# Performance work log

Measured on AMD Instinct MI355X. Metric: run time of the kernel, lower is better.

Reference implementation:

```python
import jax, jax.numpy as jnp
import numpy as np

B, S, D = 4, 2048, 768

def setup_inputs() -> dict:
    key = jax.random.key(0)
    ks = jax.random.split(key, 7)
    scale = 1.0 / np.sqrt(D)
    x = jax.random.normal(ks[0], (B, S, D), dtype=jnp.float32)
    Wq = jax.random.uniform(ks[1], (D, D), jnp.float32, -scale, scale)
    bq = jax.random.uniform(ks[2], (D,), jnp.float32, -scale, scale)
    Wk = jax.random.uniform(ks[3], (D, D), jnp.float32, -scale, scale)
    bk = jax.random.uniform(ks[4], (D,), jnp.float32, -scale, scale)
    Wv = jax.random.uniform(ks[5], (D, D), jnp.float32, -scale, scale)
    bv = jax.random.uniform(ks[6], (D,), jnp.float32, -scale, scale)
    return {"x": x, "Wq": Wq, "bq": bq, "Wk": Wk, "bk": bk, "Wv": Wv, "bv": bv}

def reference(x, Wq, bq, Wk, bk, Wv, bv):
    d = x.shape[-1]
    q = jnp.einsum('bsd,de->bse', x, Wq) + bq
    k = jnp.einsum('bsd,de->bse', x, Wk) + bk
    v = jnp.einsum('bsd,de->bse', x, Wv) + bv
    scores = jnp.einsum('bqd,bkd->bqk', q, k) / jnp.sqrt(jnp.asarray(d, x.dtype))
    attn = jax.nn.softmax(scores, axis=-1)  # [B,S,S]
    return jnp.einsum('bqk,bkd->bqd', attn, v)
```

## Files before the change

kernel.cpp:

```cpp
#include <hip/hip_runtime.h>
#include <hip/hip_bf16.h>


typedef __attribute__((ext_vector_type(8))) short short8;
typedef __attribute__((ext_vector_type(4))) short short4v;
typedef __attribute__((ext_vector_type(4))) float float4v;

static constexpr int B_ = 4, S_ = 2048, D_ = 768;
static constexpr int MS = B_ * S_;

__device__ inline short f2bf(float f) {
  __hip_bfloat16 h = __float2bfloat16(f);
  union { __hip_bfloat16 h; short s; } u; u.h = h; return u.s;
}

typedef const __attribute__((address_space(1))) unsigned int g_u32;
typedef __attribute__((address_space(3))) unsigned int l_u32;

__device__ __forceinline__ void glds16(const short* g, short* l) {
  __builtin_amdgcn_global_load_lds((g_u32*)g, (l_u32*)l, 16, 0, 0);
}

__global__ __launch_bounds__(256)
void cast_f32_bf16(const float* __restrict__ x, short* __restrict__ y, int n) {
  int i = (blockIdx.x * 256 + threadIdx.x) * 4;
  if (i + 3 < n) {
    float4v v = *(const float4v*)(x + i);
    short4v o;
    o.x = f2bf(v.x); o.y = f2bf(v.y); o.z = f2bf(v.z); o.w = f2bf(v.w);
    *(short4v*)(y + i) = o;
  }
}

__global__ void transpose_cast_w(const float* __restrict__ W0, const float* __restrict__ W1,
                                 const float* __restrict__ W2,
                                 short* __restrict__ T0, short* __restrict__ T1,
                                 short* __restrict__ T2) {
  const float* W = blockIdx.z == 0 ? W0 : (blockIdx.z == 1 ? W1 : W2);
  short* T = blockIdx.z == 0 ? T0 : (blockIdx.z == 1 ? T1 : T2);
  __shared__ float tile[32][33];
  int bx = blockIdx.x * 32, by = blockIdx.y * 32;
  int tx = threadIdx.x, ty = threadIdx.y;
  for (int r = ty; r < 32; r += 8)
    tile[r][tx] = W[(by + r) * D_ + bx + tx];
  __syncthreads();
  for (int r = ty; r < 32; r += 8)
    T[(bx + r) * D_ + by + tx] = f2bf(tile[tx][r]);
}

template<int EPI, int TM, int TN>
__global__ __launch_bounds__(256)
void gemm_bt(const short* __restrict__ A, const short* __restrict__ Bt,
             void* __restrict__ C0v, short* __restrict__ C1, short* __restrict__ C2,
             const float* __restrict__ bias0, const float* __restrict__ bias1,
             const float* __restrict__ bias2,
             int K, int lda, int ldb, int ldc,
             long sA, long sB, long sC, float scale) {
  constexpr int BMv = TM * 32, BNv = TN * 32;
  const int b = blockIdx.z;
  A += (long)b * sA;
  Bt += (long)b * sB;
  float* Cf = (float*)C0v + (long)b * sC;
  short* Cs = (short*)C0v + (long)b * sC;

  __shared__ short As[BMv * 64];
  __shared__ short Bs[BNv * 64];

  const int t = threadIdx.x;
  const int wave = t >> 6, lane = t & 63;
  const int lane16 = lane & 15, q = lane >> 4;
  const int m0 = blockIdx.y * BMv, n0 = blockIdx.x * BNv;
  const int wm = (wave >> 1) * (TM * 16), wn = (wave & 1) * (TN * 16);
  const int rsub = lane >> 3;
  const int g = (lane & 7) ^ rsub;

  auto stage = [&](int kk) {
#pragma unroll
    for (int i = wave; i < BMv / 8; i += 4)
      glds16(A + (long)(m0 + i * 8 + rsub) * lda + kk + g * 8, &As[i * 512]);
#pragma unroll
    for (int i = wave; i < BNv / 8; i += 4)
      glds16(Bt + (long)(n0 + i * 8 + rsub) * ldb + kk + g * 8, &Bs[i * 512]);
  };

  stage(0);

  float4v acc[TM][TN];
#pragma unroll
  for (int i = 0; i < TM; i++)
#pragma unroll
    for (int j = 0; j < TN; j++) acc[i][j] = {0.f, 0.f, 0.f, 0.f};

  constexpr int NRS = TM > TN ? TM : TN;
  float4v acc_rs[NRS];
#pragma unroll
  for (int i = 0; i < NRS; i++) acc_rs[i] = {0.f, 0.f, 0.f, 0.f};
  short8 ones;
#pragma unroll
  for (int e = 0; e < 8; e++) ones[e] = (short)0x3F80;

  for (int k0 = 0; k0 < K; k0 += 64) {
    __syncthreads();

    short8 af[2][TM], bfr[2][TN];
#pragma unroll
    for (int s = 0; s < 2; s++) {
#pragma unroll
      for (int i = 0; i < TM; i++) {
        int R = wm + i * 16 + lane16;
        af[s][i] = *(const short8*)&As[R * 64 + (((s * 4 + q) ^ (R & 7)) * 8)];
      }
#pragma unroll
      for (int j = 0; j < TN; j++) {
        int R = wn + j * 16 + lane16;
        bfr[s][j] = *(const short8*)&Bs[R * 64 + (((s * 4 + q) ^ (R & 7)) * 8)];
      }
    }
    __syncthreads();

    if (k0 + 64 < K) stage(k0 + 64);

#pragma unroll
    for (int s = 0; s < 2; s++) {
      if (EPI == 4) {
#pragma unroll
        for (int j = 0; j < TN; j++)
          acc_rs[j] = __builtin_amdgcn_mfma_f32_16x16x32_bf16(ones, bfr[s][j], acc_rs[j], 0, 0, 0);
      }
#pragma unroll
      for (int i = 0; i < TM; i++) {
#pragma unroll
        for (int j = 0; j < TN; j++)
          acc[i][j] = __builtin_amdgcn_mfma_f32_16x16x32_bf16(af[s][i], bfr[s][j], acc[i][j], 0, 0, 0);
      }
    }
  }

#pragma unroll
  for (int i = 0; i < TM; i++) {
    int mrow = m0 + wm + i * 16 + q * 4;
    if (EPI == 0) {
#pragma unroll
      for (int j = 0; j < TN; j++) {
        int ncol = n0 + wn + j * 16 + lane16;
        if (ncol < 1536) {
          short* dst = ncol < 768 ? Cs : C1;
          const float* bs = ncol < 768 ? bias0 : bias1;
          int c = ncol < 768 ? ncol : ncol - 768;
#pragma unroll
          for (int rr = 0; rr < 4; rr++)
            dst[(long)(mrow + rr) * 768 + c] = f2bf(acc[i][j][rr] + bs[c]);
        } else {
          int e = ncol - 1536;
          float bv = bias2[e];
          short4v o;
#pragma unroll
          for (int rr = 0; rr < 4; rr++) o[rr] = f2bf(acc[i][j][rr] + bv);
          *(short4v*)&C2[(long)e * MS + mrow] = o;
        }
      }
    } else {
#pragma unroll
      for (int j = 0; j < TN; j++) {
        int ncol = n0 + wn + j * 16 + lane16;
        float inv = 1.0f / acc_rs[j][0];
        float4v o;
#pragma unroll
        for (int rr = 0; rr < 4; rr++) o[rr] = acc[i][j][rr] * inv;
        *(float4v*)&Cf[(long)ncol * ldc + mrow] = o;
      }
    }
  }
}

template<int EPI>
__global__ __launch_bounds__(512, 2)
void gemm8p(const short* __restrict__ A, const short* __restrict__ Bt,
            void* __restrict__ C0v, short* __restrict__ C1, short* __restrict__ C2,
            const float* __restrict__ bias0, const float* __restrict__ bias1,
            const float* __restrict__ bias2,
            int K, int lda, int ldb, int ldc,
            long sA, long sB, long sC, float scale) {
  const int b = blockIdx.z;
  A += (long)b * sA;
  Bt += (long)b * sB;
  short* Cs = (short*)C0v + (long)b * sC;

  __shared__ short As[2][256 * 64];
  __shared__ short Bs[2][256 * 64];

  const int t = threadIdx.x;
  const int wave = t >> 6, lane = t & 63;
  const int lane16 = lane & 15, q = lane >> 4;
  const int xr = lane16 & 7;
  const int m0 = blockIdx.y * 256, n0 = blockIdx.x * 256;
  const int wm = (wave >> 2) * 128, wn = (wave & 3) * 64;
  const int rsub = lane >> 3;
  const int g = (lane & 7) ^ rsub;
  const int nt = K >> 6;

  auto stageA = [&](int u, int tt) {
    short* dst = &As[tt & 1][0];
    const short* src = A + tt * 64 + g * 8;
#pragma unroll
    for (int r = 0; r < 2; r++) {
      int row0 = u * 64 + r * 128 + wave * 8;
      glds16(src + (long)(m0 + row0 + rsub) * lda, dst + row0 * 64);
    }
  };
  auto stageB = [&](int u, int tt) {
    short* dst = &Bs[tt & 1][0];
    const short* src = Bt + tt * 64 + g * 8;
#pragma unroll
    for (int r = 0; r < 2; r++) {
      int idx = r * 8 + wave;
      int row0 = (idx >> 2) * 64 + u * 32 + (idx & 3) * 8;
      glds16(src + (long)(n0 + row0 + rsub) * ldb, dst + row0 * 64);
    }
  };

  float4v acc[8][4];
#pragma unroll
  for (int i = 0; i < 8; i++)
#pragma unroll
    for (int j = 0; j < 4; j++) acc[i][j] = {0.f, 0.f, 0.f, 0.f};

  stageA(0, 0); stageA(1, 0); stageB(0, 0); stageB(1, 0);
  if (nt > 1) { stageA(0, 1); stageB(0, 1); stageA(1, 1); }
  if (nt > 1) asm volatile("s_waitcnt vmcnt(6)" ::: "memory");
  else        asm volatile("s_waitcnt vmcnt(0)" ::: "memory");
  __builtin_amdgcn_s_barrier();

#pragma unroll 2
  for (int tt = 0; tt < nt; ++tt) {
    const short* Ab = &As[tt & 1][0];
    const short* Bb = &Bs[tt & 1][0];
    short8 a[4][2], b0[2][2], b1[2][2];

#pragma unroll
    for (int ii = 0; ii < 4; ii++) {
      int R = wm + ii * 16 + lane16;
#pragma unroll
      for (int s = 0; s < 2; s++)
        a[ii][s] = *(const short8*)&Ab[R * 64 + (((s * 4 + q) ^ xr) * 8)];
    }
#pragma unroll
    for (int jj = 0; jj < 2; jj++) {
      int R = wn + jj * 16 + lane16;
#pragma unroll
      for (int s = 0; s < 2; s++)
        b0[jj][s] = *(const short8*)&Bb[R * 64 + (((s * 4 + q) ^ xr) * 8)];
    }
    if (tt + 1 < nt) stageB(1, tt + 1);
    __builtin_amdgcn_s_barrier();
    asm volatile("s_waitcnt lgkmcnt(0)" ::: "memory");
    __builtin_amdgcn_sched_barrier(0);
    __builtin_amdgcn_s_setprio(1);
#pragma unroll
    for (int s = 0; s < 2; s++)
#pragma unroll
      for (int ii = 0; ii < 4; ii++)
#pragma unroll
        for (int jj = 0; jj < 2; jj++)
          acc[ii][jj] = __builtin_amdgcn_mfma_f32_16x16x32_bf16(a[ii][s], b0[jj][s], acc[ii][jj], 0, 0, 0);
    __builtin_amdgcn_s_setprio(0);
    __builtin_amdgcn_s_barrier();

#pragma unroll
    for (int jj = 0; jj < 2; jj++) {
      int R = wn + 32 + jj * 16 + lane16;
#pragma unroll
      for (int s = 0; s < 2; s++)
        b1[jj][s] = *(const short8*)&Bb[R * 64 + (((s * 4 + q) ^ xr) * 8)];
    }
    if (tt + 2 < nt) stageA(0, tt + 2);
    __builtin_amdgcn_s_barrier();
    asm volatile("s_waitcnt lgkmcnt(0)" ::: "memory");
    __builtin_amdgcn_sched_barrier(0);
    __builtin_amdgcn_s_setprio(1);
#pragma unroll
    for (int s = 0; s < 2; s++)
#pragma unroll
      for (int ii = 0; ii < 4; ii++)
#pragma unroll
        for (int jj = 0; jj < 2; jj++)
          acc[ii][2 + jj] = __builtin_amdgcn_mfma_f32_16x16x32_bf16(a[ii][s], b1[jj][s], acc[ii][2 + jj], 0, 0, 0);
    __builtin_amdgcn_s_setprio(0);
    __builtin_amdgcn_s_barrier();

#pragma unroll
    for (int ii = 0; ii < 4; ii++) {
      int R = wm + 64 + ii * 16 + lane16;
#pragma unroll
      for (int s = 0; s < 2; s++)
        a[ii][s] = *(const short8*)&Ab[R * 64 + (((s * 4 + q) ^ xr) * 8)];
    }
    if (tt + 2 < nt) stageB(0, tt + 2);
    __builtin_amdgcn_s_barrier();
    asm volatile("s_waitcnt lgkmcnt(0)" ::: "memory");
    __builtin_amdgcn_sched_barrier(0);
    __builtin_amdgcn_s_setprio(1);
#pragma unroll
    for (int s = 0; s < 2; s++)
#pragma unroll
      for (int ii = 0; ii < 4; ii++)
#pragma unroll
        for (int jj = 0; jj < 2; jj++)
          acc[4 + ii][2 + jj] = __builtin_amdgcn_mfma_f32_16x16x32_bf16(a[ii][s], b1[jj][s], acc[4 + ii][2 + jj], 0, 0, 0);
    __builtin_amdgcn_s_setprio(0);
    __builtin_amdgcn_s_barrier();

    if (tt + 2 < nt) stageA(1, tt + 2);
    __builtin_amdgcn_s_barrier();
    __builtin_amdgcn_s_setprio(1);
#pragma unroll
    for (int s = 0; s < 2; s++)
#pragma unroll
      for (int ii = 0; ii < 4; ii++)
#pragma unroll
        for (int jj = 0; jj < 2; jj++)
          acc[4 + ii][jj] = __builtin_amdgcn_mfma_f32_16x16x32_bf16(a[ii][s], b0[jj][s], acc[4 + ii][jj], 0, 0, 0);
    __builtin_amdgcn_s_setprio(0);
    if (tt + 2 < nt) asm volatile("s_waitcnt vmcnt(6)" ::: "memory");
    else             asm volatile("s_waitcnt vmcnt(0)" ::: "memory");
    __builtin_amdgcn_s_barrier();
  }

#pragma unroll
  for (int i = 0; i < 8; i++) {
    int mrow = m0 + wm + i * 16 + q * 4;
#pragma unroll
    for (int j = 0; j < 4; j++) {
      int ncol = n0 + wn + j * 16 + lane16;
#pragma unroll
      for (int rr = 0; rr < 4; rr++)
        Cs[(long)(mrow + rr) * ldc + ncol] = f2bf(__expf(acc[i][j][rr] * scale));
    }
  }
}

extern "C" void kernel_launch(void* const* d_in, const int* in_sizes, int n_in,
                              void* d_out, int out_size, void* d_ws, size_t ws_size,
                              hipStream_t stream) {
  const float* x  = (const float*)d_in[0];
  const float* Wq = (const float*)d_in[1];
  const float* bq = (const float*)d_in[2];
  const float* Wk = (const float*)d_in[3];
  const float* bk = (const float*)d_in[4];
  const float* Wv = (const float*)d_in[5];
  const float* bv = (const float*)d_in[6];
  float* out = (float*)d_out;

  short* Xb  = (short*)d_ws;
  short* WqT = Xb + (long)MS * D_;
  short* WkT = WqT + (long)D_ * D_;
  short* WvT = WkT + (long)D_ * D_;
  short* Qb  = WvT + (long)D_ * D_;
  short* Kb  = Qb + (long)MS * D_;
  short* Vt  = Kb + (long)MS * D_;
  short* Es  = Vt + (long)MS * D_;

  cast_f32_bf16<<<(MS * D_) / 1024, 256, 0, stream>>>(x, Xb, MS * D_);
  transpose_cast_w<<<dim3(24, 24, 3), dim3(32, 8), 0, stream>>>(Wq, Wk, Wv, WqT, WkT, WvT);

  gemm_bt<0, 4, 4><<<dim3(2304 / 128, MS / 128, 1), 256, 0, stream>>>(
      Xb, WqT, Qb, Kb, Vt, bq, bk, bv,
      D_, D_, D_, D_, 0, 0, 0, 1.0f);
  gemm8p<2><<<dim3(S_ / 256, S_ / 256, B_), 512, 0, stream>>>(
      Qb, Kb, Es, nullptr, nullptr, nullptr, nullptr, nullptr,
      D_, D_, D_, S_,
      (long)S_ * D_, (long)S_ * D_, (long)S_ * S_, 1.0f / sqrtf((float)D_));
  gemm_bt<4, 4, 4><<<dim3(S_ / 128, D_ / 128, B_), 256, 0, stream>>>(
      Vt, Es, out, nullptr, nullptr, nullptr, nullptr, nullptr,
      S_, MS, S_, D_,
      (long)S_, (long)S_ * S_, (long)S_ * D_, 1.0f);
}
```

Measured before the change: 196.5 us.

## Run PV GEMM on 256x256 pipelined kernel with split-K and combine pass

Replaces the 128x128 gemm_bt for the attention-times-V product with the 8-wave 256x256 pipelined gemm8p kernel. The key dimension is split in two halves across blockIdx.z to raise block count, and each half writes fp32 partials and row sums. A new pv_combine kernel adds the halves and normalizes by the summed row sums. This trades an extra fp32 partial buffer round-trip and an extra launch for higher MFMA efficiency in the big GEMM.

```diff
diff --git a/kernel.cpp b/kernel.cpp
--- a/kernel.cpp
+++ b/kernel.cpp
@@ -48,6 +48,20 @@
     T[(bx + r) * D_ + by + tx] = f2bf(tile[tx][r]);
 }
 
+__global__ __launch_bounds__(256)
+void pv_combine(const float* __restrict__ p1, const float* __restrict__ rs,
+                float* __restrict__ out) {
+  long i = ((long)blockIdx.x * 256 + threadIdx.x) * 4;
+  long qg = i / 768;
+  float inv = 1.0f / (rs[qg] + rs[8192 + qg]);
+  float4v a = *(const float4v*)(out + i);
+  float4v p = *(const float4v*)(p1 + i);
+  float4v o;
+#pragma unroll
+  for (int r = 0; r < 4; r++) o[r] = (a[r] + p[r]) * inv;
+  *(float4v*)(out + i) = o;
+}
+
 template<int EPI, int TM, int TN>
 __global__ __launch_bounds__(256)
 void gemm_bt(const short* __restrict__ A, const short* __restrict__ Bt,
@@ -60,7 +74,6 @@
   const int b = blockIdx.z;
   A += (long)b * sA;
   Bt += (long)b * sB;
-  float* Cf = (float*)C0v + (long)b * sC;
   short* Cs = (short*)C0v + (long)b * sC;
 
   __shared__ short As[BMv * 64];
@@ -91,14 +104,6 @@
 #pragma unroll
     for (int j = 0; j < TN; j++) acc[i][j] = {0.f, 0.f, 0.f, 0.f};
 
-  constexpr int NRS = TM > TN ? TM : TN;
-  float4v acc_rs[NRS];
-#pragma unroll
-  for (int i = 0; i < NRS; i++) acc_rs[i] = {0.f, 0.f, 0.f, 0.f};
-  short8 ones;
-#pragma unroll
-  for (int e = 0; e < 8; e++) ones[e] = (short)0x3F80;
-
   for (int k0 = 0; k0 < K; k0 += 64) {
     __syncthreads();
 
@@ -122,11 +127,6 @@
 
 #pragma unroll
     for (int s = 0; s < 2; s++) {
-      if (EPI == 4) {
-#pragma unroll
-        for (int j = 0; j < TN; j++)
-          acc_rs[j] = __builtin_amdgcn_mfma_f32_16x16x32_bf16(ones, bfr[s][j], acc_rs[j], 0, 0, 0);
-      }
 #pragma unroll
       for (int i = 0; i < TM; i++) {
 #pragma unroll
@@ -139,35 +139,23 @@
 #pragma unroll
   for (int i = 0; i < TM; i++) {
     int mrow = m0 + wm + i * 16 + q * 4;
-    if (EPI == 0) {
-#pragma unroll
-      for (int j = 0; j < TN; j++) {
-        int ncol = n0 + wn + j * 16 + lane16;
-        if (ncol < 1536) {
-          short* dst = ncol < 768 ? Cs : C1;
-          const float* bs = ncol < 768 ? bias0 : bias1;
-          int c = ncol < 768 ? ncol : ncol - 768;
-#pragma unroll
-          for (int rr = 0; rr < 4; rr++)
-            dst[(long)(mrow + rr) * 768 + c] = f2bf(acc[i][j][rr] + bs[c]);
-        } else {
-          int e = ncol - 1536;
-          float bv = bias2[e];
-          short4v o;
-#pragma unroll
-          for (int rr = 0; rr < 4; rr++) o[rr] = f2bf(acc[i][j][rr] + bv);
-          *(short4v*)&C2[(long)e * MS + mrow] = o;
-        }
-      }
-    } else {
-#pragma unroll
-      for (int j = 0; j < TN; j++) {
-        int ncol = n0 + wn + j * 16 + lane16;
-        float inv = 1.0f / acc_rs[j][0];
-        float4v o;
-#pragma unroll
-        for (int rr = 0; rr < 4; rr++) o[rr] = acc[i][j][rr] * inv;
-        *(float4v*)&Cf[(long)ncol * ldc + mrow] = o;
+#pragma unroll
+    for (int j = 0; j < TN; j++) {
+      int ncol = n0 + wn + j * 16 + lane16;
+      if (ncol < 1536) {
+        short* dst = ncol < 768 ? Cs : C1;
+        const float* bs = ncol < 768 ? bias0 : bias1;
+        int c = ncol < 768 ? ncol : ncol - 768;
+#pragma unroll
+        for (int rr = 0; rr < 4; rr++)
+          dst[(long)(mrow + rr) * 768 + c] = f2bf(acc[i][j][rr] + bs[c]);
+      } else {
+        int e = ncol - 1536;
+        float bv = bias2[e];
+        short4v o;
+#pragma unroll
+        for (int rr = 0; rr < 4; rr++) o[rr] = f2bf(acc[i][j][rr] + bv);
+        *(short4v*)&C2[(long)e * MS + mrow] = o;
       }
     }
   }
@@ -181,9 +169,10 @@
             const float* __restrict__ bias2,
             int K, int lda, int ldb, int ldc,
             long sA, long sB, long sC, float scale) {
-  const int b = blockIdx.z;
-  A += (long)b * sA;
-  Bt += (long)b * sB;
+  int b = blockIdx.z, hh = 0;
+  if (EPI == 5) { hh = b & 1; b >>= 1; }
+  A += (long)b * sA + (EPI == 5 ? hh * 1024 : 0);
+  Bt += (long)b * sB + (EPI == 5 ? hh * 1024 : 0);
   short* Cs = (short*)C0v + (long)b * sC;
 
   __shared__ short As[2][256 * 64];
@@ -225,6 +214,13 @@
 #pragma unroll
     for (int j = 0; j < 4; j++) acc[i][j] = {0.f, 0.f, 0.f, 0.f};
 
+  float4v acc_rs[4];
+#pragma unroll
+  for (int j = 0; j < 4; j++) acc_rs[j] = {0.f, 0.f, 0.f, 0.f};
+  short8 ones;
+#pragma unroll
+  for (int e = 0; e < 8; e++) ones[e] = (short)0x3F80;
+
   stageA(0, 0); stageA(1, 0); stageB(0, 0); stageB(1, 0);
   if (nt > 1) { stageA(0, 1); stageB(0, 1); stageA(1, 1); }
   if (nt > 1) asm volatile("s_waitcnt vmcnt(6)" ::: "memory");
@@ -263,6 +259,13 @@
 #pragma unroll
         for (int jj = 0; jj < 2; jj++)
           acc[ii][jj] = __builtin_amdgcn_mfma_f32_16x16x32_bf16(a[ii][s], b0[jj][s], acc[ii][jj], 0, 0, 0);
+    if (EPI == 5) {
+#pragma unroll
+      for (int s = 0; s < 2; s++)
+#pragma unroll
+        for (int jj = 0; jj < 2; jj++)
+          acc_rs[jj] = __builtin_amdgcn_mfma_f32_16x16x32_bf16(ones, b0[jj][s], acc_rs[jj], 0, 0, 0);
+    }
     __builtin_amdgcn_s_setprio(0);
     __builtin_amdgcn_s_barrier();
 
@@ -285,6 +288,13 @@
 #pragma unroll
         for (int jj = 0; jj < 2; jj++)
           acc[ii][2 + jj] = __builtin_amdgcn_mfma_f32_16x16x32_bf16(a[ii][s], b1[jj][s], acc[ii][2 + jj], 0, 0, 0);
+    if (EPI == 5) {
+#pragma unroll
+      for (int s = 0; s < 2; s++)
+#pragma unroll
+        for (int jj = 0; jj < 2; jj++)
+          acc_rs[2 + jj] = __builtin_amdgcn_mfma_f32_16x16x32_bf16(ones, b1[jj][s], acc_rs[2 + jj], 0, 0, 0);
+    }
     __builtin_amdgcn_s_setprio(0);
     __builtin_amdgcn_s_barrier();
 
@@ -326,15 +336,36 @@
     __builtin_amdgcn_s_barrier();
   }
 
-#pragma unroll
-  for (int i = 0; i < 8; i++) {
-    int mrow = m0 + wm + i * 16 + q * 4;
-#pragma unroll
-    for (int j = 0; j < 4; j++) {
-      int ncol = n0 + wn + j * 16 + lane16;
-#pragma unroll
-      for (int rr = 0; rr < 4; rr++)
-        Cs[(long)(mrow + rr) * ldc + ncol] = f2bf(__expf(acc[i][j][rr] * scale));
+  if (EPI == 2) {
+#pragma unroll
+    for (int i = 0; i < 8; i++) {
+      int mrow = m0 + wm + i * 16 + q * 4;
+#pragma unroll
+      for (int j = 0; j < 4; j++) {
+        int ncol = n0 + wn + j * 16 + lane16;
+#pragma unroll
+        for (int rr = 0; rr < 4; rr++)
+          Cs[(long)(mrow + rr) * ldc + ncol] = f2bf(__expf(acc[i][j][rr] * scale));
+      }
+    }
+  } else {
+    float* dst = (hh ? (float*)C1 : (float*)C0v) + (long)b * S_ * 768;
+    float* rsb = (float*)C2 + (long)hh * 8192 + (long)b * 2048;
+    if (wm == 0 && q == 0) {
+#pragma unroll
+      for (int j = 0; j < 4; j++) {
+        int ncol = n0 + wn + j * 16 + lane16;
+        rsb[ncol] = acc_rs[j][0];
+      }
+    }
+#pragma unroll
+    for (int i = 0; i < 8; i++) {
+      int mrow = m0 + wm + i * 16 + q * 4;
+#pragma unroll
+      for (int j = 0; j < 4; j++) {
+        int ncol = n0 + wn + j * 16 + lane16;
+        *(float4v*)&dst[(long)ncol * ldc + mrow] = acc[i][j];
+      }
     }
   }
 }
@@ -360,6 +391,9 @@
   short* Vt  = Kb + (long)MS * D_;
   short* Es  = Vt + (long)MS * D_;
 
+  float* p1f = (float*)d_ws;
+  float* rsf = p1f + (long)MS * D_;
+
   cast_f32_bf16<<<(MS * D_) / 1024, 256, 0, stream>>>(x, Xb, MS * D_);
   transpose_cast_w<<<dim3(24, 24, 3), dim3(32, 8), 0, stream>>>(Wq, Wk, Wv, WqT, WkT, WvT);
 
@@ -370,8 +404,9 @@
       Qb, Kb, Es, nullptr, nullptr, nullptr, nullptr, nullptr,
       D_, D_, D_, S_,
       (long)S_ * D_, (long)S_ * D_, (long)S_ * S_, 1.0f / sqrtf((float)D_));
-  gemm_bt<4, 4, 4><<<dim3(S_ / 128, D_ / 128, B_), 256, 0, stream>>>(
-      Vt, Es, out, nullptr, nullptr, nullptr, nullptr, nullptr,
-      S_, MS, S_, D_,
-      (long)S_, (long)S_ * S_, (long)S_ * D_, 1.0f);
-}
+  gemm8p<5><<<dim3(S_ / 256, D_ / 256, B_ * 2), 512, 0, stream>>>(
+      Vt, Es, out, (short*)p1f, (short*)rsf, nullptr, nullptr, nullptr,
+      1024, MS, S_, D_,
+      (long)S_, (long)S_ * S_, 0, 1.0f);
+  pv_combine<<<(MS * D_) / 1024, 256, 0, stream>>>(p1f, rsf, out);
+}
```

New measurement: 216.7 us. +10.3%, slower.
